# Optimization experiments

Measured on AMD Instinct MI355X. Metric: run time of the kernel, lower is better.

Reference implementation:

```python
import jax, jax.numpy as jnp
import numpy as np

S, L = 512, 32            # number of sequences, max sequence length
IN_FEATURES = 13824       # 512*3*3 + 1024*3*3 ROI features
HID = 1024                # Head.hidden_dim
LSTM_H = HID // 2         # per-direction hidden size (bidirectional)
N_CLASSES = 4787
BN_EPS = 1e-5


def _make_ragged():
    lengths = (4 + (np.arange(S) % 29)).astype(np.int32)  # 4..32, sum = 9121
    n = int(lengths.sum())
    perm = np.random.RandomState(0).permutation(n).astype(np.int32)
    seq_idx = np.zeros((S, L), dtype=np.int32)
    off = 0
    for i, l in enumerate(lengths):
        seq_idx[i, :l] = perm[off:off + l]
        off += l
    return n, jnp.asarray(seq_idx), jnp.asarray(lengths)


def setup_inputs() -> dict:
    n, seq_idx, lengths = _make_ragged()
    key = jax.random.key(0)
    ks = jax.random.split(key, 16)
    w = lambda k, shp, s=0.02: (jax.random.normal(k, shp, dtype=jnp.float32) * s)
    return {
        "x": jax.random.normal(ks[0], (n, IN_FEATURES), dtype=jnp.float32),
        "fc1_w": w(ks[1], (HID, IN_FEATURES)),
        "fc1_b": w(ks[2], (HID,)),
        "bn_gamma": jnp.ones((HID,), jnp.float32),
        "bn_beta": jnp.zeros((HID,), jnp.float32),
        "fc2_w": w(ks[3], (N_CLASSES, HID)),
        "fc2_b": w(ks[4], (N_CLASSES,)),
        "w_ih_f": w(ks[5], (4 * LSTM_H, HID)),
        "w_hh_f": w(ks[6], (4 * LSTM_H, LSTM_H)),
        "b_ih_f": w(ks[7], (4 * LSTM_H,)),
        "b_hh_f": w(ks[8], (4 * LSTM_H,)),
        "w_ih_b": w(ks[9], (4 * LSTM_H, HID)),
        "w_hh_b": w(ks[10], (4 * LSTM_H, LSTM_H)),
        "b_ih_b": w(ks[11], (4 * LSTM_H,)),
        "b_hh_b": w(ks[12], (4 * LSTM_H,)),
        "seq_idx": seq_idx,
        "lengths": lengths,
    }


def _lstm_scan(seq_x, w_ih, w_hh, b_ih, b_hh):
    # seq_x: [S, L, HID] -> outputs [S, L, LSTM_H]; PyTorch gate order i,f,g,o
    s = seq_x.shape[0]
    h0 = jnp.zeros((s, LSTM_H), seq_x.dtype)
    c0 = jnp.zeros((s, LSTM_H), seq_x.dtype)
    x_gates = jnp.einsum('slh,gh->slg', seq_x, w_ih) + b_ih + b_hh  # precompute input gates

    def step(carry, xg):
        h, c = carry
        g = xg + h @ w_hh.T
        i, f, gg, o = jnp.split(g, 4, axis=-1)
        c = jax.nn.sigmoid(f) * c + jax.nn.sigmoid(i) * jnp.tanh(gg)
        h = jax.nn.sigmoid(o) * jnp.tanh(c)
        return (h, c), h

    _, hs = jax.lax.scan(step, (h0, c0), x_gates.transpose(1, 0, 2))  # [L, S, H]
    return hs.transpose(1, 0, 2)


def reference(x, fc1_w, fc1_b, bn_gamma, bn_beta, fc2_w, fc2_b,
              w_ih_f, w_hh_f, b_ih_f, b_hh_f,
              w_ih_b, w_hh_b, b_ih_b, b_hh_b,
              seq_idx, lengths):
    n = x.shape[0]
    # Head: fc1 -> relu -> BatchNorm1d (training-mode batch stats)
    h = jax.nn.relu(x @ fc1_w.T + fc1_b)
    mean = h.mean(axis=0)
    var = jnp.mean((h - mean) ** 2, axis=0)
    feats = (h - mean) * jax.lax.rsqrt(var + BN_EPS) * bn_gamma + bn_beta  # [N, HID]

    # ragged gather into packed [S, L, HID]
    mask = jnp.arange(L)[None, :] < lengths[:, None]          # [S, L]
    gidx = jnp.where(mask, seq_idx, 0)
    seq_x = feats[gidx] * mask[:, :, None]                    # zero padded slots

    # forward direction (padding at tail: harmless to causal scan)
    hf = _lstm_scan(seq_x, w_ih_f, w_hh_f, b_ih_f, b_hh_f)
    # backward direction: reverse each sequence within its valid length
    rev = jnp.clip(lengths[:, None] - 1 - jnp.arange(L)[None, :], 0, L - 1)  # [S, L]
    seq_rev = jnp.take_along_axis(seq_x, rev[:, :, None], axis=1)
    hb_rev = _lstm_scan(seq_rev, w_ih_b, w_hh_b, b_ih_b, b_hh_b)
    hb = jnp.take_along_axis(hb_rev, rev[:, :, None], axis=1)  # un-reverse (involution on valid region)

    out = jnp.concatenate([hf, hb], axis=-1)                   # [S, L, HID]

    # scatter back to flat roi order; padded slots dropped out-of-bounds
    sidx = jnp.where(mask, seq_idx, n).reshape(-1)
    lstm_feats = jnp.zeros((n, HID), feats.dtype).at[sidx].set(
        out.reshape(-1, HID), mode='drop')

    logits = lstm_feats @ fc2_w.T + fc2_b                      # apply_fc_out
    return logits
```

## Files before the change

### kernel.cpp

```cpp
#include <hip/hip_runtime.h>

typedef short short8v __attribute__((ext_vector_type(8)));
typedef float f32x4 __attribute__((ext_vector_type(4)));

__device__ __forceinline__ unsigned short f2bf(float f){
  unsigned int u = __float_as_uint(f);
  u += 0x7fffu + ((u >> 16) & 1u);
  return (unsigned short)(u >> 16);
}
__device__ __forceinline__ float bf2f(unsigned short h){
  return __uint_as_float(((unsigned int)h) << 16);
}
union H2F { unsigned short u; _Float16 h; };
__device__ __forceinline__ float fp16f(unsigned short b){ H2F t; t.u = b; return (float)t.h; }

typedef __attribute__((address_space(1))) const unsigned int gu32;
typedef __attribute__((address_space(3))) unsigned int lu32;
__device__ __forceinline__ void gl16(const void* g, void* l){
  __builtin_amdgcn_global_load_lds((gu32*)g, (lu32*)l, 16, 0, 0);
}

template<int EPI>
__global__ __launch_bounds__(256)
void gemm16(const unsigned short* __restrict__ A, const unsigned short* __restrict__ B,
            void* __restrict__ Cout, int M, int N, int K, int lda, int ldb, int ldc,
            const float* __restrict__ bias)
{
  __shared__ __align__(16) unsigned short As[128 * 64];
  __shared__ __align__(16) unsigned short Bs[128 * 64];

  const int tid = threadIdx.x;
  const int gx = gridDim.x;
  const int nwg = gx * gridDim.y;
  int dd = blockIdx.y * gx + blockIdx.x;
  int q = nwg >> 3, r = nwg & 7, xc = dd & 7, t8 = dd >> 3;
  int Lid = (xc < r ? xc * (q + 1) : r * (q + 1) + (xc - r) * q) + t8;
  const int bcol = (Lid % gx) * 128;
  const int brow = (Lid / gx) * 128;

  const int l = tid & 63, w = tid >> 6;
  const int wr = (w >> 1) * 64, wc = (w & 1) * 64;
  const int r16 = l & 15, kg = l >> 4;
  const int swzl = (l & 7) * 8;
  const int stg_off = (((l & 7) ^ (l >> 3)) * 8);
  const int srow = l >> 3;

  f32x4 acc[4][4];
  #pragma unroll
  for (int m = 0; m < 4; m++)
    #pragma unroll
    for (int nn = 0; nn < 4; nn++) { f32x4 z = {0.f, 0.f, 0.f, 0.f}; acc[m][nn] = z; }

  const int kz = blockIdx.z * K;
  const unsigned short* Ab0 = A + (size_t)brow * lda + kz;
  const unsigned short* Bb0 = B + (size_t)bcol * ldb + kz;

  auto stage = [&](int k0) {
    #pragma unroll
    for (int i = 0; i < 4; i++) {
      int chunk = w * 4 + i;
      gl16(Ab0 + (size_t)(chunk * 8 + srow) * lda + k0 + stg_off, As + chunk * 512);
      gl16(Bb0 + (size_t)(chunk * 8 + srow) * ldb + k0 + stg_off, Bs + chunk * 512);
    }
  };

  const int nk = K >> 6;
  for (int kt = 0; kt < nk; kt++) {
    stage(kt << 6);
    __syncthreads();
    #pragma unroll
    for (int kk = 0; kk < 2; kk++) {
      short8v af[4], bfv[4];
      #pragma unroll
      for (int m = 0; m < 4; m++)
        af[m] = *(const short8v*)(As + (wr + m * 16 + r16) * 64 + ((kk * 32 + kg * 8) ^ swzl));
      #pragma unroll
      for (int nn = 0; nn < 4; nn++)
        bfv[nn] = *(const short8v*)(Bs + (wc + nn * 16 + r16) * 64 + ((kk * 32 + kg * 8) ^ swzl));
      #pragma unroll
      for (int m = 0; m < 4; m++)
        #pragma unroll
        for (int nn = 0; nn < 4; nn++)
          acc[m][nn] = __builtin_amdgcn_mfma_f32_16x16x32_bf16(af[m], bfv[nn], acc[m][nn], 0, 0, 0);
    }
    __syncthreads();
  }

  float* Cz = (float*)Cout + (EPI == 4 ? (size_t)blockIdx.z * M * ldc : 0);

  #pragma unroll
  for (int m = 0; m < 4; m++) {
    int row0 = brow + wr + m * 16 + kg * 4;
    #pragma unroll
    for (int nn = 0; nn < 4; nn++) {
      int col = bcol + wc + nn * 16 + r16;
      if (col < N) {
        float b = (EPI == 4) ? 0.f : bias[col];
        #pragma unroll
        for (int rr = 0; rr < 4; rr++) {
          int row = row0 + rr;
          if (row < M) {
            float val = acc[m][nn][rr] + b;
            if (EPI == 3) {
              int dL = col >> 11, rc = col & 2047;
              int cg = rc >> 6, g = (rc >> 4) & 3, u = rc & 15;
              int pc = (dL << 11) + (((cg << 4) + u) << 2) + g;
              ((_Float16*)Cout)[(size_t)row * ldc + pc] = (_Float16)val;
            }
            else Cz[(size_t)row * ldc + col] = val;
          }
        }
      }
    }
  }
}

__global__ __launch_bounds__(256) void fc1_reduce(const float* __restrict__ P, const float* __restrict__ bias,
                                                  unsigned short* __restrict__ h, float* __restrict__ part,
                                                  int n, int mpad) {
  int b = blockIdx.x, tid = threadIdx.x;
  int c0 = tid * 4;
  float4 bsv = *(const float4*)(bias + c0);
  float s[4] = {0,0,0,0}, qq[4] = {0,0,0,0};
  int rbeg = b * 32;
  for (int r = rbeg; r < rbeg + 32; r++) {
    float4 a = *(const float4*)(P + (size_t)r * 1024 + c0);
    float4 bq = *(const float4*)(P + (size_t)(mpad + r) * 1024 + c0);
    float v0 = fmaxf(a.x + bq.x + bsv.x, 0.f);
    float v1 = fmaxf(a.y + bq.y + bsv.y, 0.f);
    float v2 = fmaxf(a.z + bq.z + bsv.z, 0.f);
    float v3 = fmaxf(a.w + bq.w + bsv.w, 0.f);
    if (r < n) {
      s[0] += v0; qq[0] += v0 * v0;
      s[1] += v1; qq[1] += v1 * v1;
      s[2] += v2; qq[2] += v2 * v2;
      s[3] += v3; qq[3] += v3 * v3;
    }
    *(ushort4*)(h + (size_t)r * 1024 + c0) = make_ushort4(f2bf(v0), f2bf(v1), f2bf(v2), f2bf(v3));
  }
  float* pp = part + (size_t)b * 2048;
  #pragma unroll
  for (int k = 0; k < 4; k++) { pp[(c0 + k) * 2] = s[k]; pp[(c0 + k) * 2 + 1] = qq[k]; }
}

__global__ __launch_bounds__(256, 1)
void lstm_persist(const unsigned short* __restrict__ whhc, const unsigned short* __restrict__ bcp,
                  const _Float16* __restrict__ G,
                  const int* __restrict__ gf, const int* __restrict__ gb, const int* __restrict__ sb,
                  unsigned short* __restrict__ hst,
                  unsigned short* __restrict__ lfeat, int* __restrict__ flags)
{
  __shared__ __align__(16) unsigned short Bsh[64 * 512];
  const int tid = threadIdx.x;
  const int l = tid & 63, w = tid >> 6;
  const int b = blockIdx.x;
  const int d = (b >> 2) & 1;
  const int rg = b & 3;
  const int c = b >> 3;
  const int grp = b & 7;
  const int rowbase = d * 512 + rg * 128;
  const int r16 = l & 15, kg = l >> 4;
  const int swzl = (r16 & 7) * 8;
  const int hu = c * 16 + r16;

  const unsigned short* Bsrc = whhc + ((size_t)(d * 2048 + c * 64)) * 512;
  #pragma unroll
  for (int i = 0; i < 16; i++) {
    int rr = w * 16 + i;
    gl16(Bsrc + (size_t)rr * 512 + ((l * 8) ^ ((rr & 7) * 8)), Bsh + rr * 512);
  }
  asm volatile("s_waitcnt vmcnt(0)");
  __syncthreads();

  float creg[2][4];
  #pragma unroll
  for (int m = 0; m < 2; m++)
    #pragma unroll
    for (int rr = 0; rr < 4; rr++) creg[m][rr] = 0.f;

  for (int t = 0; t < 32; t++) {
    ushort4 gv[2][4];
    int scv[2][4];
    #pragma unroll
    for (int m = 0; m < 2; m++) {
      #pragma unroll
      for (int rr = 0; rr < 4; rr++) {
        int row = rowbase + w * 32 + m * 16 + kg * 4 + rr;
        int sq = row & 511;
        int gi = d ? gb[sq * 32 + t] : gf[sq * 32 + t];
        const unsigned short* src = (gi >= 0)
            ? (const unsigned short*)G + ((size_t)gi * 4096 + (d << 11) + hu * 4)
            : bcp + ((d << 11) + hu * 4);
        gv[m][rr] = *(const ushort4*)src;
        scv[m][rr] = d ? sb[sq * 32 + t] : gi;
      }
    }

    if (t > 0) {
      while (true) {
        int fv = 0x7fffffff;
        if (l < 32)
          fv = __hip_atomic_load(flags + ((grp * 32 + l) << 5), __ATOMIC_RELAXED, __HIP_MEMORY_SCOPE_AGENT);
        if (__all(fv >= t)) break;
        __builtin_amdgcn_s_sleep(1);
      }
    }
    asm volatile("" ::: "memory");

    const unsigned short* hp = hst + (size_t)(t & 1) * (1024 * 512);
    unsigned short* hn = hst + (size_t)((t + 1) & 1) * (1024 * 512);

    short8v av[2][16];
    #pragma unroll
    for (int m = 0; m < 2; m++) {
      unsigned long long a64 = (unsigned long long)(hp + (size_t)(rowbase + w * 32 + m * 16 + r16) * 512 + kg * 8);
      #pragma unroll
      for (int kf = 0; kf < 16; kf++) {
        asm volatile("global_load_dwordx4 %0, %1, off offset:%c2 sc0 sc1"
                     : "=v"(av[m][kf]) : "v"(a64), "i"(kf * 64) : "memory");
      }
    }
    asm volatile("s_waitcnt vmcnt(0)" ::: "memory");

    f32x4 acc[2][4];
    #pragma unroll
    for (int m = 0; m < 2; m++)
      #pragma unroll
      for (int nn = 0; nn < 4; nn++) { f32x4 z = {0.f, 0.f, 0.f, 0.f}; acc[m][nn] = z; }

    #pragma unroll
    for (int kc = 0; kc < 8; kc++) {
      short8v bv[4][2];
      #pragma unroll
      for (int nn = 0; nn < 4; nn++)
        #pragma unroll
        for (int kk = 0; kk < 2; kk++)
          bv[nn][kk] = *(const short8v*)(Bsh + (nn * 16 + r16) * 512 + ((kc * 64 + kk * 32 + kg * 8) ^ swzl));
      #pragma unroll
      for (int kk = 0; kk < 2; kk++)
        #pragma unroll
        for (int m = 0; m < 2; m++)
          #pragma unroll
          for (int nn = 0; nn < 4; nn++)
            acc[m][nn] = __builtin_amdgcn_mfma_f32_16x16x32_bf16(av[m][kc * 2 + kk], bv[nn][kk], acc[m][nn], 0, 0, 0);
    }

    #pragma unroll
    for (int m = 0; m < 2; m++) {
      #pragma unroll
      for (int reg = 0; reg < 4; reg++) {
        int row = rowbase + w * 32 + m * 16 + kg * 4 + reg;
        float g_i = acc[m][0][reg] + fp16f(gv[m][reg].x);
        float g_f = acc[m][1][reg] + fp16f(gv[m][reg].y);
        float g_g = acc[m][2][reg] + fp16f(gv[m][reg].z);
        float g_o = acc[m][3][reg] + fp16f(gv[m][reg].w);
        float si = 1.f / (1.f + __expf(-g_i));
        float sf = 1.f / (1.f + __expf(-g_f));
        float so = 1.f / (1.f + __expf(-g_o));
        float cn = sf * creg[m][reg] + si * tanhf(g_g);
        float hnv = so * tanhf(cn);
        creg[m][reg] = cn;
        unsigned int hb = f2bf(hnv);
        unsigned long long ha = (unsigned long long)(hn + (size_t)row * 512 + hu);
        asm volatile("global_store_short %0, %1, off sc0 sc1" :: "v"(ha), "v"(hb) : "memory");
        int sc = scv[m][reg];
        if (sc >= 0) lfeat[(size_t)sc * 1024 + d * 512 + hu] = f2bf(hnv);
      }
    }

    __syncthreads();
    if (t < 31 && tid == 0)
      __hip_atomic_store(flags + ((grp * 32 + c) << 5), t + 1, __ATOMIC_RELAXED, __HIP_MEMORY_SCOPE_AGENT);
  }
}

__global__ __launch_bounds__(256) void conv_bf16(const float* __restrict__ src, unsigned short* __restrict__ dst,
                                                 size_t nvalid, size_t total) {
  size_t stride = (size_t)gridDim.x * 2048;
  for (size_t i = ((size_t)blockIdx.x * 256 + threadIdx.x) * 8; i < total; i += stride) {
    unsigned short o[8];
    if (i + 8 <= nvalid) {
      float4 a = *(const float4*)(src + i);
      float4 b = *(const float4*)(src + i + 4);
      o[0] = f2bf(a.x); o[1] = f2bf(a.y); o[2] = f2bf(a.z); o[3] = f2bf(a.w);
      o[4] = f2bf(b.x); o[5] = f2bf(b.y); o[6] = f2bf(b.z); o[7] = f2bf(b.w);
    } else {
      #pragma unroll
      for (int j = 0; j < 8; j++) o[j] = (i + j < nvalid) ? f2bf(src[i + j]) : (unsigned short)0;
    }
    *(ushort4*)(dst + i) = make_ushort4(o[0], o[1], o[2], o[3]);
    *(ushort4*)(dst + i + 4) = make_ushort4(o[4], o[5], o[6], o[7]);
  }
}

__global__ __launch_bounds__(256) void bn_final(const float* __restrict__ part, const float* __restrict__ gamma,
                                                const float* __restrict__ beta, float* __restrict__ scale,
                                                float* __restrict__ shift, int M, int nb) {
  int c = blockIdx.x * 256 + threadIdx.x;
  float s = 0.f, q = 0.f;
  for (int b = 0; b < nb; b++) { s += part[(size_t)b * 2048 + c * 2]; q += part[(size_t)b * 2048 + c * 2 + 1]; }
  float mean = s / (float)M;
  float var = q / (float)M - mean * mean;
  float sc = gamma[c] * rsqrtf(var + 1e-5f);
  scale[c] = sc; shift[c] = beta[c] - mean * sc;
}

__global__ __launch_bounds__(256) void prep_tables(const int* __restrict__ seq_idx, const int* __restrict__ lengths,
                                                   int* __restrict__ gf, int* __restrict__ gb, int* __restrict__ sb) {
  int idx = blockIdx.x * 256 + threadIdx.x;
  if (idx < 512 * 32) {
    int s = idx >> 5, t = idx & 31;
    int len = lengths[s];
    gf[idx] = (t < len) ? seq_idx[idx] : -1;
    int rb = len - 1 - t;
    gb[idx] = seq_idx[(s << 5) + (rb < 0 ? 0 : rb)];
    sb[idx] = (t < len) ? seq_idx[(s << 5) + (len - 1 - t)] : -1;
  }
}

__global__ __launch_bounds__(256) void build_wih(const float* __restrict__ wf, const float* __restrict__ wb,
                                                 const float* __restrict__ bihf, const float* __restrict__ bhhf,
                                                 const float* __restrict__ bihb, const float* __restrict__ bhhb,
                                                 const float* __restrict__ scale, const float* __restrict__ shift,
                                                 unsigned short* __restrict__ wcdst, float* __restrict__ bc,
                                                 _Float16* __restrict__ bcp) {
  int orow = blockIdx.x * 4 + (threadIdx.x >> 6);
  int l = threadIdx.x & 63;
  int dir = orow >> 11, j = orow & 2047;
  int cc = j >> 6, jj = j & 63, g = jj >> 4, u = jj & 15;
  int srow = g * 512 + cc * 16 + u;
  const float* src = (dir ? wb : wf) + (size_t)srow * 1024;
  unsigned short* dst = wcdst + (size_t)orow * 1024;
  float sacc = 0.f;
  #pragma unroll
  for (int jv = 0; jv < 16; jv++) {
    int k = l + jv * 64;
    float v = src[k];
    sacc += shift[k] * v;
    dst[k] = f2bf(v * scale[k]);
  }
  #pragma unroll
  for (int o2 = 32; o2 > 0; o2 >>= 1) sacc += __shfl_down(sacc, o2);
  if (l == 0) {
    float bb = (dir ? (bihb[srow] + bhhb[srow]) : (bihf[srow] + bhhf[srow])) + sacc;
    bc[orow] = bb;
    int pc = (dir << 11) + (((cc << 4) + u) << 2) + g;
    bcp[pc] = (_Float16)bb;
  }
}

__global__ __launch_bounds__(256) void build_whh(const float* __restrict__ wf, const float* __restrict__ wb,
                                                 unsigned short* __restrict__ o) {
  int cidx = blockIdx.x * 256 + threadIdx.x;
  if (cidx < 4096 * 64) {
    int orow = cidx >> 6, k0 = (cidx & 63) * 8;
    int dir = orow >> 11, j = orow & 2047;
    int cc = j >> 6, jj = j & 63, g = jj >> 4, u = jj & 15;
    const float* src = (dir ? wb : wf) + (size_t)(g * 512 + cc * 16 + u) * 512 + k0;
    unsigned short* dst = o + (size_t)orow * 512 + k0;
    float4 a = *(const float4*)(src);
    float4 bq = *(const float4*)(src + 4);
    dst[0] = f2bf(a.x); dst[1] = f2bf(a.y); dst[2] = f2bf(a.z); dst[3] = f2bf(a.w);
    dst[4] = f2bf(bq.x); dst[5] = f2bf(bq.y); dst[6] = f2bf(bq.z); dst[7] = f2bf(bq.w);
  }
}

extern "C" void kernel_launch(void* const* d_in, const int* in_sizes, int n_in,
                              void* d_out, int out_size, void* d_ws, size_t ws_size,
                              hipStream_t stream) {
  const float* x     = (const float*)d_in[0];
  const float* fc1w  = (const float*)d_in[1];
  const float* fc1b  = (const float*)d_in[2];
  const float* gamma = (const float*)d_in[3];
  const float* beta  = (const float*)d_in[4];
  const float* fc2w  = (const float*)d_in[5];
  const float* fc2b  = (const float*)d_in[6];
  const float* wihf  = (const float*)d_in[7];
  const float* whhf  = (const float*)d_in[8];
  const float* bihf  = (const float*)d_in[9];
  const float* bhhf  = (const float*)d_in[10];
  const float* wihb  = (const float*)d_in[11];
  const float* whhb  = (const float*)d_in[12];
  const float* bihb  = (const float*)d_in[13];
  const float* bhhb  = (const float*)d_in[14];
  const int* seq_idx = (const int*)d_in[15];
  const int* lengths = (const int*)d_in[16];
  float* out = (float*)d_out;

  const int n = in_sizes[0] / 13824;
  const int mb = (n + 127) / 128;
  const int mpad = mb * 128;

  char* ws = (char*)d_ws;
  size_t off = 0;
  auto alloc = [&](size_t bytes) -> void* {
    void* p = ws + off; off += (bytes + 255) & ~(size_t)255; return p;
  };
  unsigned short* x_h  = (unsigned short*)alloc((size_t)mpad * 13824 * 2);
  unsigned short* w1_h = (unsigned short*)alloc((size_t)1024 * 13824 * 2);
  unsigned short* w2_h = (unsigned short*)alloc((size_t)4864 * 1024 * 2);
  unsigned short* h    = (unsigned short*)alloc((size_t)mpad * 1024 * 2);
  _Float16*       G    = (_Float16*)alloc((size_t)mpad * 4096 * 2);
  unsigned short* wihc = (unsigned short*)alloc((size_t)4096 * 1024 * 2);
  unsigned short* whhc = (unsigned short*)alloc((size_t)4096 * 512 * 2);
  float* bias_c = (float*)alloc(4096 * 4);
  _Float16* bias_p = (_Float16*)alloc(4096 * 2);
  unsigned short* lfeat  = (unsigned short*)alloc((size_t)mpad * 1024 * 2);
  unsigned short* hstate = (unsigned short*)alloc((size_t)2 * 1024 * 512 * 2);
  float* part   = (float*)alloc((size_t)(mpad / 32) * 2048 * 4);
  float* scale  = (float*)alloc(1024 * 4);
  float* shift  = (float*)alloc(1024 * 4);
  int* gf  = (int*)alloc(16384 * 4);
  int* gb  = (int*)alloc(16384 * 4);
  int* sb  = (int*)alloc(16384 * 4);
  int* flags = (int*)alloc(256 * 32 * 4);

  float* P = (float*)G;

  dim3 blk(256);

  conv_bf16<<<2048, blk, 0, stream>>>(x, x_h, (size_t)n * 13824, (size_t)mpad * 13824);
  conv_bf16<<<1024, blk, 0, stream>>>(fc1w, w1_h, (size_t)1024 * 13824, (size_t)1024 * 13824);
  conv_bf16<<<256, blk, 0, stream>>>(fc2w, w2_h, (size_t)4787 * 1024, (size_t)4864 * 1024);
  build_whh<<<1024, blk, 0, stream>>>(whhf, whhb, whhc);
  prep_tables<<<64, blk, 0, stream>>>(seq_idx, lengths, gf, gb, sb);
  hipMemsetAsync(hstate, 0, (size_t)2 * 1024 * 512 * 2, stream);
  hipMemsetAsync(flags, 0, 256 * 32 * 4, stream);

  gemm16<4><<<dim3(8, mb, 2), blk, 0, stream>>>(
      x_h, w1_h, P, mpad, 1024, 6912, 13824, 13824, 1024, nullptr);

  fc1_reduce<<<mpad / 32, blk, 0, stream>>>(P, fc1b, h, part, n, mpad);
  bn_final<<<4, blk, 0, stream>>>(part, gamma, beta, scale, shift, n, mpad / 32);
  build_wih<<<1024, blk, 0, stream>>>(wihf, wihb, bihf, bhhf, bihb, bhhb, scale, shift, wihc, bias_c, bias_p);

  gemm16<3><<<dim3(32, mb), blk, 0, stream>>>(
      h, wihc, G, n, 4096, 1024, 1024, 1024, 4096, bias_c);

  lstm_persist<<<256, blk, 0, stream>>>(whhc, (const unsigned short*)bias_p, G, gf, gb, sb,
                                        hstate, lfeat, flags);

  gemm16<0><<<dim3(38, mb), blk, 0, stream>>>(
      lfeat, w2_h, out, n, 4787, 1024, 1024, 1024, 4787, fc2b);
}
```

Baseline: 1.224 ms.

## Replace 128x128 GEMM with double-buffered 256x256 8-wave pipelined kernel

```diff
diff --git a/kernel.cpp b/kernel.cpp
--- a/kernel.cpp
+++ b/kernel.cpp
@@ -2,6 +2,7 @@
 
 typedef short short8v __attribute__((ext_vector_type(8)));
 typedef float f32x4 __attribute__((ext_vector_type(4)));
+typedef _Float16 h4v __attribute__((ext_vector_type(4)));
 
 __device__ __forceinline__ unsigned short f2bf(float f){
   unsigned int u = __float_as_uint(f);
@@ -21,93 +22,135 @@
 }
 
 template<int EPI>
-__global__ __launch_bounds__(256)
-void gemm16(const unsigned short* __restrict__ A, const unsigned short* __restrict__ B,
-            void* __restrict__ Cout, int M, int N, int K, int lda, int ldb, int ldc,
-            const float* __restrict__ bias)
+__global__ __launch_bounds__(512, 2)
+void gemm256(const unsigned short* __restrict__ A, const unsigned short* __restrict__ B,
+             void* __restrict__ Cout, int M, int N, int K, int lda, int ldb, int ldc,
+             const float* __restrict__ bias)
 {
-  __shared__ __align__(16) unsigned short As[128 * 64];
-  __shared__ __align__(16) unsigned short Bs[128 * 64];
+  __shared__ __align__(16) unsigned short As[2 * 2 * 256 * 32];
+  __shared__ __align__(16) unsigned short Bs[2 * 2 * 256 * 32];
 
   const int tid = threadIdx.x;
   const int gx = gridDim.x;
   const int nwg = gx * gridDim.y;
   int dd = blockIdx.y * gx + blockIdx.x;
-  int q = nwg >> 3, r = nwg & 7, xc = dd & 7, t8 = dd >> 3;
-  int Lid = (xc < r ? xc * (q + 1) : r * (q + 1) + (xc - r) * q) + t8;
-  const int bcol = (Lid % gx) * 128;
-  const int brow = (Lid / gx) * 128;
+  int q8 = nwg >> 3, r8 = nwg & 7, xc = dd & 7, t8 = dd >> 3;
+  int Lid = (xc < r8 ? xc * (q8 + 1) : r8 * (q8 + 1) + (xc - r8) * q8) + t8;
+  const int bcol = (Lid % gx) * 256;
+  const int brow = (Lid / gx) * 256;
 
   const int l = tid & 63, w = tid >> 6;
-  const int wr = (w >> 1) * 64, wc = (w & 1) * 64;
+  const int wr = w >> 2;
+  const int wn = w & 3;
   const int r16 = l & 15, kg = l >> 4;
-  const int swzl = (l & 7) * 8;
-  const int stg_off = (((l & 7) ^ (l >> 3)) * 8);
-  const int srow = l >> 3;
-
-  f32x4 acc[4][4];
-  #pragma unroll
-  for (int m = 0; m < 4; m++)
+  const int swz = (r16 >> 1) & 3;
+  const int srow4 = l >> 2, sblk = l & 3;
+  const int scol = (sblk ^ ((l >> 3) & 3)) * 8;
+
+  const int kz = blockIdx.z * K;
+  const unsigned short* Ag = A + (size_t)(brow + w * 32 + srow4) * lda + kz + scol;
+  const unsigned short* Bg = B + (size_t)(bcol + w * 32 + srow4) * ldb + kz + scol;
+  unsigned short* Asd = As + w * 1024;
+  unsigned short* Bsd = Bs + w * 1024;
+
+#define STA(buf, kh, kt) do { \
+    gl16(Ag + (size_t)(kt) * 64 + (kh) * 32, Asd + (buf) * 16384 + (kh) * 8192); \
+    gl16(Ag + (size_t)(kt) * 64 + (kh) * 32 + (size_t)16 * lda, Asd + (buf) * 16384 + (kh) * 8192 + 512); \
+  } while (0)
+#define STB(buf, kh, kt) do { \
+    gl16(Bg + (size_t)(kt) * 64 + (kh) * 32, Bsd + (buf) * 16384 + (kh) * 8192); \
+    gl16(Bg + (size_t)(kt) * 64 + (kh) * 32 + (size_t)16 * ldb, Bsd + (buf) * 16384 + (kh) * 8192 + 512); \
+  } while (0)
+
+  const unsigned short* Ard = As + (wr * 128 + r16) * 32 + ((kg ^ swz) * 8);
+  const unsigned short* Brd = Bs + (wn * 64 + r16) * 32 + ((kg ^ swz) * 8);
+
+  f32x4 acc[8][4];
+  #pragma unroll
+  for (int m = 0; m < 8; m++)
     #pragma unroll
     for (int nn = 0; nn < 4; nn++) { f32x4 z = {0.f, 0.f, 0.f, 0.f}; acc[m][nn] = z; }
 
-  const int kz = blockIdx.z * K;
-  const unsigned short* Ab0 = A + (size_t)brow * lda + kz;
-  const unsigned short* Bb0 = B + (size_t)bcol * ldb + kz;
-
-  auto stage = [&](int k0) {
-    #pragma unroll
-    for (int i = 0; i < 4; i++) {
-      int chunk = w * 4 + i;
-      gl16(Ab0 + (size_t)(chunk * 8 + srow) * lda + k0 + stg_off, As + chunk * 512);
-      gl16(Bb0 + (size_t)(chunk * 8 + srow) * ldb + k0 + stg_off, Bs + chunk * 512);
-    }
-  };
+  short8v af[4], bfr[4];
+
+#define LDA4(c, kk, mq) { \
+    _Pragma("unroll") for (int i = 0; i < 4; i++) \
+      af[i] = *(const short8v*)(Ard + (c) * 16384 + (kk) * 8192 + ((mq) * 4 + i) * 512); }
+#define LDB4(c, kk) { \
+    _Pragma("unroll") for (int nn = 0; nn < 4; nn++) \
+      bfr[nn] = *(const short8v*)(Brd + (c) * 16384 + (kk) * 8192 + nn * 512); }
+#define MFMAQ(mq) { \
+    __builtin_amdgcn_s_setprio(1); \
+    _Pragma("unroll") for (int i = 0; i < 4; i++) { \
+      _Pragma("unroll") for (int nn = 0; nn < 4; nn++) \
+        acc[(mq) * 4 + i][nn] = __builtin_amdgcn_mfma_f32_16x16x32_bf16(af[i], bfr[nn], acc[(mq) * 4 + i][nn], 0, 0, 0); \
+    } \
+    __builtin_amdgcn_s_setprio(0); }
 
   const int nk = K >> 6;
-  for (int kt = 0; kt < nk; kt++) {
-    stage(kt << 6);
-    __syncthreads();
-    #pragma unroll
-    for (int kk = 0; kk < 2; kk++) {
-      short8v af[4], bfv[4];
-      #pragma unroll
-      for (int m = 0; m < 4; m++)
-        af[m] = *(const short8v*)(As + (wr + m * 16 + r16) * 64 + ((kk * 32 + kg * 8) ^ swzl));
-      #pragma unroll
-      for (int nn = 0; nn < 4; nn++)
-        bfv[nn] = *(const short8v*)(Bs + (wc + nn * 16 + r16) * 64 + ((kk * 32 + kg * 8) ^ swzl));
-      #pragma unroll
-      for (int m = 0; m < 4; m++)
-        #pragma unroll
-        for (int nn = 0; nn < 4; nn++)
-          acc[m][nn] = __builtin_amdgcn_mfma_f32_16x16x32_bf16(af[m], bfv[nn], acc[m][nn], 0, 0, 0);
-    }
-    __syncthreads();
-  }
-
-  float* Cz = (float*)Cout + (EPI == 4 ? (size_t)blockIdx.z * M * ldc : 0);
-
-  #pragma unroll
-  for (int m = 0; m < 4; m++) {
-    int row0 = brow + wr + m * 16 + kg * 4;
+  STA(0, 0, 0); STB(0, 0, 0); STA(0, 1, 0); STB(0, 1, 0);
+  asm volatile("s_waitcnt vmcnt(4)" ::: "memory");
+  __builtin_amdgcn_s_barrier();
+  __builtin_amdgcn_sched_barrier(0);
+
+  for (int j = 0; j < nk; j++) {
+    const int c = j & 1, nb = c ^ 1;
+    const bool pf = (j + 1 < nk);
+    LDB4(c, 0); LDA4(c, 0, 0);
+    if (pf) STA(nb, 0, j + 1);
+    __builtin_amdgcn_s_barrier();
+    MFMAQ(0);
+    __builtin_amdgcn_s_barrier();
+    LDA4(c, 0, 1);
+    if (pf) STB(nb, 0, j + 1);
+    __builtin_amdgcn_s_barrier();
+    MFMAQ(1);
+    if (pf) asm volatile("s_waitcnt vmcnt(4)" ::: "memory");
+    else    asm volatile("s_waitcnt vmcnt(0)" ::: "memory");
+    __builtin_amdgcn_s_barrier();
+    __builtin_amdgcn_sched_barrier(0);
+    LDB4(c, 1); LDA4(c, 1, 0);
+    if (pf) STA(nb, 1, j + 1);
+    __builtin_amdgcn_s_barrier();
+    MFMAQ(0);
+    __builtin_amdgcn_s_barrier();
+    LDA4(c, 1, 1);
+    if (pf) STB(nb, 1, j + 1);
+    __builtin_amdgcn_s_barrier();
+    MFMAQ(1);
+    if (pf) asm volatile("s_waitcnt vmcnt(4)" ::: "memory");
+    __builtin_amdgcn_s_barrier();
+    __builtin_amdgcn_sched_barrier(0);
+  }
+#undef STA
+#undef STB
+#undef LDA4
+#undef LDB4
+#undef MFMAQ
+
+  #pragma unroll
+  for (int m = 0; m < 8; m++) {
+    const int row0 = brow + wr * 128 + m * 16 + kg * 4;
     #pragma unroll
     for (int nn = 0; nn < 4; nn++) {
-      int col = bcol + wc + nn * 16 + r16;
+      const int col = bcol + wn * 64 + nn * 16 + r16;
       if (col < N) {
-        float b = (EPI == 4) ? 0.f : bias[col];
+        const float bv = (EPI == 5) ? 0.f : bias[col];
         #pragma unroll
         for (int rr = 0; rr < 4; rr++) {
-          int row = row0 + rr;
+          const int row = row0 + rr;
           if (row < M) {
-            float val = acc[m][nn][rr] + b;
+            float val = acc[m][nn][rr] + bv;
             if (EPI == 3) {
               int dL = col >> 11, rc = col & 2047;
               int cg = rc >> 6, g = (rc >> 4) & 3, u = rc & 15;
               int pc = (dL << 11) + (((cg << 4) + u) << 2) + g;
               ((_Float16*)Cout)[(size_t)row * ldc + pc] = (_Float16)val;
+            } else if (EPI == 5) {
+              ((_Float16*)Cout)[(size_t)blockIdx.z * M * ldc + (size_t)row * ldc + col] = (_Float16)val;
+            } else {
+              ((float*)Cout)[(size_t)row * ldc + col] = val;
             }
-            else Cz[(size_t)row * ldc + col] = val;
           }
         }
       }
@@ -115,7 +158,7 @@
   }
 }
 
-__global__ __launch_bounds__(256) void fc1_reduce(const float* __restrict__ P, const float* __restrict__ bias,
+__global__ __launch_bounds__(256) void fc1_reduce(const _Float16* __restrict__ P, const float* __restrict__ bias,
                                                   unsigned short* __restrict__ h, float* __restrict__ part,
                                                   int n, int mpad) {
   int b = blockIdx.x, tid = threadIdx.x;
@@ -124,12 +167,13 @@
   float s[4] = {0,0,0,0}, qq[4] = {0,0,0,0};
   int rbeg = b * 32;
   for (int r = rbeg; r < rbeg + 32; r++) {
-    float4 a = *(const float4*)(P + (size_t)r * 1024 + c0);
-    float4 bq = *(const float4*)(P + (size_t)(mpad + r) * 1024 + c0);
-    float v0 = fmaxf(a.x + bq.x + bsv.x, 0.f);
-    float v1 = fmaxf(a.y + bq.y + bsv.y, 0.f);
-    float v2 = fmaxf(a.z + bq.z + bsv.z, 0.f);
-    float v3 = fmaxf(a.w + bq.w + bsv.w, 0.f);
+    h4v a0 = *(const h4v*)(P + (size_t)r * 1024 + c0);
+    h4v a1 = *(const h4v*)(P + ((size_t)mpad + r) * 1024 + c0);
+    h4v a2 = *(const h4v*)(P + ((size_t)2 * mpad + r) * 1024 + c0);
+    float v0 = fmaxf((float)a0[0] + (float)a1[0] + (float)a2[0] + bsv.x, 0.f);
+    float v1 = fmaxf((float)a0[1] + (float)a1[1] + (float)a2[1] + bsv.y, 0.f);
+    float v2 = fmaxf((float)a0[2] + (float)a1[2] + (float)a2[2] + bsv.z, 0.f);
+    float v3 = fmaxf((float)a0[3] + (float)a1[3] + (float)a2[3] + bsv.w, 0.f);
     if (r < n) {
       s[0] += v0; qq[0] += v0 * v0;
       s[1] += v1; qq[1] += v1 * v1;
@@ -388,8 +432,8 @@
   float* out = (float*)d_out;
 
   const int n = in_sizes[0] / 13824;
-  const int mb = (n + 127) / 128;
-  const int mpad = mb * 128;
+  const int mt = (n + 255) / 256;
+  const int mpad = mt * 256;
 
   char* ws = (char*)d_ws;
   size_t off = 0;
@@ -415,9 +459,10 @@
   int* sb  = (int*)alloc(16384 * 4);
   int* flags = (int*)alloc(256 * 32 * 4);
 
-  float* P = (float*)G;
+  _Float16* P16 = (_Float16*)G;
 
   dim3 blk(256);
+  dim3 blk5(512);
 
   conv_bf16<<<2048, blk, 0, stream>>>(x, x_h, (size_t)n * 13824, (size_t)mpad * 13824);
   conv_bf16<<<1024, blk, 0, stream>>>(fc1w, w1_h, (size_t)1024 * 13824, (size_t)1024 * 13824);
@@ -427,19 +472,19 @@
   hipMemsetAsync(hstate, 0, (size_t)2 * 1024 * 512 * 2, stream);
   hipMemsetAsync(flags, 0, 256 * 32 * 4, stream);
 
-  gemm16<4><<<dim3(8, mb, 2), blk, 0, stream>>>(
-      x_h, w1_h, P, mpad, 1024, 6912, 13824, 13824, 1024, nullptr);
-
-  fc1_reduce<<<mpad / 32, blk, 0, stream>>>(P, fc1b, h, part, n, mpad);
+  gemm256<5><<<dim3(4, mt, 3), blk5, 0, stream>>>(
+      x_h, w1_h, P16, mpad, 1024, 4608, 13824, 13824, 1024, nullptr);
+
+  fc1_reduce<<<mpad / 32, blk, 0, stream>>>(P16, fc1b, h, part, n, mpad);
   bn_final<<<4, blk, 0, stream>>>(part, gamma, beta, scale, shift, n, mpad / 32);
   build_wih<<<1024, blk, 0, stream>>>(wihf, wihb, bihf, bhhf, bihb, bhhb, scale, shift, wihc, bias_c, bias_p);
 
-  gemm16<3><<<dim3(32, mb), blk, 0, stream>>>(
+  gemm256<3><<<dim3(16, mt), blk5, 0, stream>>>(
       h, wihc, G, n, 4096, 1024, 1024, 1024, 4096, bias_c);
 
   lstm_persist<<<256, blk, 0, stream>>>(whhc, (const unsigned short*)bias_p, G, gf, gb, sb,
                                         hstate, lfeat, flags);
 
-  gemm16<0><<<dim3(38, mb), blk, 0, stream>>>(
+  gemm256<0><<<dim3(19, mt), blk5, 0, stream>>>(
       lfeat, w2_h, out, n, 4787, 1024, 1024, 1024, 4787, fc2b);
 }
```

Result: no change. 1.241 ms (+1.4%).
